# Kernel optimization log

Hardware: AMD Instinct MI355X
Metric: run time of the kernel (lower is better)

Reference implementation:

```python
import jax, jax.numpy as jnp
import numpy as np

P = 256        # number of graph pairs
LMAX = 32      # max graph size (padded to LMAX+1 incl. virtual node)
F = 2048       # num_input_features
E = 256        # embedding_dim
INF = 10000.0


def _lengths():
    i = np.arange(P)
    len_s = 8 + (i % 25)
    len_t = 8 + ((7 * i + 3) % 25)
    return len_s.astype(np.int32), len_t.astype(np.int32)


def setup_inputs() -> dict:
    key = jax.random.key(0)
    ks = jax.random.split(key, 6)
    len_s_np, len_t_np = _lengths()
    Ns, Nt = int(len_s_np.sum()), int(len_t_np.sum())
    x_s = jax.random.normal(ks[0], (Ns, F), jnp.float32)
    x_t = jax.random.normal(ks[1], (Nt, F), jnp.float32)
    W1 = jax.random.normal(ks[2], (E, F), jnp.float32) / np.float32(np.sqrt(F))
    b1 = jnp.zeros((E,), jnp.float32)
    W2 = jax.random.normal(ks[3], (E, E), jnp.float32) / np.float32(np.sqrt(E))
    b2 = jnp.zeros((E,), jnp.float32)
    virtual_embedding = jax.random.uniform(ks[4], (F,), jnp.float32)
    return {"x_s": x_s, "x_t": x_t, "W1": W1, "b1": b1, "W2": W2, "b2": b2,
            "virtual_embedding": virtual_embedding,
            "len_s": jnp.asarray(len_s_np), "len_t": jnp.asarray(len_t_np)}


def _embed(x, W1, b1, W2, b2):
    # nn.Sequential(Linear, Dropout(eval=identity), ReLU, Linear, ReLU)
    h = jax.nn.relu(x @ W1.T + b1)
    return jax.nn.relu(h @ W2.T + b2)


def _safe_cdist(a, b):
    # a: [P,L,E], b: [P,L,E] -> [P,L,L] Euclidean, grad-safe at 0
    sq = (jnp.sum(a * a, -1)[:, :, None] + jnp.sum(b * b, -1)[:, None, :]
          - 2.0 * jnp.einsum('pid,pjd->pij', a, b))
    sq = jnp.maximum(sq, 0.0)
    pos = sq > 0
    return jnp.where(pos, jnp.sqrt(jnp.where(pos, sq, 1.0)), 0.0)


def _pad_embed(emb, virtual_e, lens):
    # ragged [N,E] -> padded [P,LMAX+1,E]; slot lens[p] (and beyond) = virtual
    pos = jnp.arange(LMAX + 1)
    off = jnp.cumsum(lens) - lens                       # exclusive prefix sum
    idx = off[:, None] + jnp.minimum(pos[None, :], lens[:, None] - 1)
    mask = pos[None, :] < lens[:, None]
    return jnp.where(mask[..., None], emb[idx], virtual_e[None, None, :])


def _edit_costs(x_s, x_t, W1, b1, W2, b2, virtual_embedding, len_s, len_t):
    emb_s = _embed(x_s, W1, b1, W2, b2)
    emb_t = _embed(x_t, W1, b1, W2, b2)
    ve = _embed(virtual_embedding[None, :], W1, b1, W2, b2)[0]
    A = _pad_embed(emb_s, ve, len_s)                    # [P,L+1,E]
    B = _pad_embed(emb_t, ve, len_t)
    d = _safe_cdist(A, B)                               # [P,L+1,L+1]
    pos = jnp.arange(LMAX + 1)
    valid = ((pos[None, :, None] <= len_s[:, None, None]) &
             (pos[None, None, :] <= len_t[:, None, None]))
    tot = jnp.sum(jnp.where(valid, d, 0.0), axis=(1, 2))
    scale = (len_s * len_t).astype(d.dtype) / tot
    return jnp.where(valid, d * scale[:, None, None], 0.0), valid


def _lap_jv(C):
    # Jonker-Volgenant / e-maxx Hungarian for square cost matrix; returns col of each row
    C = np.asarray(C, dtype=np.float64)
    n = C.shape[0]
    u = np.zeros(n + 1)
    v = np.zeros(n + 1)
    p = np.zeros(n + 1, dtype=np.int64)
    way = np.zeros(n + 1, dtype=np.int64)
    for i in range(1, n + 1):
        p[0] = i
        j0 = 0
        minv = np.full(n + 1, np.inf)
        used = np.zeros(n + 1, dtype=bool)
        while True:
            used[j0] = True
            i0 = p[j0]
            cur = C[i0 - 1, :] - u[i0] - v[1:]
            upd = (~used[1:]) & (cur < minv[1:])
            minv[1:][upd] = cur[upd]
            way[1:][upd] = j0
            masked = np.where(used[1:], np.inf, minv[1:])
            j1 = int(np.argmin(masked)) + 1
            delta = masked[j1 - 1]
            u[p[used]] += delta
            v[used] -= delta
            minv[1:][~used[1:]] -= delta
            j0 = j1
            if p[j0] == 0:
                break
        while j0:
            j1 = way[j0]
            p[j0] = p[j1]
            j0 = j1
    row_of_col = p[1:] - 1
    col_of_row = np.empty(n, dtype=np.int64)
    col_of_row[row_of_col] = np.arange(n)
    return col_of_row


def _lsape_align(ec, n, m):
    # LSAPE expansion identical to GEDModelHomology.lsape
    N = n + m
    C = np.zeros((N, N))
    C[:n, :m] = ec[:n, :m]
    C[n:, :m] = INF
    C[:n, m:] = INF
    C[np.arange(n, n + m), np.arange(m)] = ec[n, :m]
    C[np.arange(n), np.arange(m, m + n)] = ec[:n, m]
    C[~np.isfinite(C)] = INF
    p = _lap_jv(C)
    q = np.arange(N)
    align = np.zeros((n + 1, m + 1), dtype=np.int32)
    align[np.minimum(q, n), np.minimum(p, m)] = 1
    align[-1, -1] = 0
    return align


def _alignments(costs_np, len_s_np, len_t_np):
    out = np.zeros((costs_np.shape[0], LMAX + 1, LMAX + 1), dtype=np.int32)
    for pr in range(costs_np.shape[0]):
        n, m = int(len_s_np[pr]), int(len_t_np[pr])
        out[pr, :n + 1, :m + 1] = _lsape_align(costs_np[pr, :n + 1, :m + 1], n, m)
    return out


def reference(x_s, x_t, W1, b1, W2, b2, virtual_embedding, len_s, len_t):
    costs, _ = _edit_costs(x_s, x_t, W1, b1, W2, b2, virtual_embedding, len_s, len_t)
    aligns = jnp.asarray(_alignments(np.asarray(costs),
                                     np.asarray(len_s), np.asarray(len_t)))
    geds = (jnp.sum(aligns.astype(costs.dtype) * costs, axis=(1, 2))
            / (len_s + len_t).astype(costs.dtype))
    return aligns, costs, geds
```

## Files before the change

kernel.cpp:

```cpp
#include <hip/hip_runtime.h>
#include <math.h>

#define LMAXP1 33
#define EDIM   256
#define FBIG   3.0e38f

typedef _Float16 half8 __attribute__((ext_vector_type(8)));
typedef float    f32x4 __attribute__((ext_vector_type(4)));

__device__ inline unsigned pk2h(_Float16 a, _Float16 b) {
    union { _Float16 h[2]; unsigned u; } q; q.h[0] = a; q.h[1] = b; return q.u;
}

__global__ __launch_bounds__(256)
void k_convw(const float* __restrict__ W, unsigned* __restrict__ Wh,
             unsigned* __restrict__ Wl, int npairs) {
    const int stride = gridDim.x * blockDim.x;
    for (int i = blockIdx.x * blockDim.x + threadIdx.x; i < npairs; i += stride) {
        const float a0 = W[2*i] * 1024.0f, a1 = W[2*i+1] * 1024.0f;
        const _Float16 h0 = (_Float16)a0, h1 = (_Float16)a1;
        const _Float16 l0 = (_Float16)(a0 - (float)h0);
        const _Float16 l1 = (_Float16)(a1 - (float)h1);
        Wh[i] = pk2h(h0, h1); Wl[i] = pk2h(l0, l1);
    }
}

#define ASTR 20
__global__ __launch_bounds__(256)
void k_gemm_splitk(const float* __restrict__ S0, int n0,
                   const float* __restrict__ S1, int n1,
                   const float* __restrict__ S2,
                   const unsigned* __restrict__ Wh, const unsigned* __restrict__ Wl,
                   float* __restrict__ Part, int Mtot, int K, int kchunk) {
    __shared__ alignas(16) unsigned AsH[64 * ASTR],  AsL[64 * ASTR];
    __shared__ alignas(16) unsigned BsH[256 * ASTR], BsL[256 * ASTR];
    const int tid = threadIdx.x;
    const int m0  = blockIdx.x * 64;
    const int ks  = blockIdx.z;
    const int kb  = ks * kchunk;
    const int ke  = (kb + kchunk < K) ? kb + kchunk : K;

    const int sar = tid >> 2, sak = (tid & 3) << 3;
    const int gr  = m0 + sar;
    const float* srow = nullptr;
    if (gr < n0)            srow = S0 + (size_t)gr * K;
    else if (gr < n0 + n1)  srow = S1 + (size_t)(gr - n0) * K;
    else if (gr < Mtot)     srow = S2;

    const int lane = tid & 63, wv = tid >> 6;
    const int wc = wv << 6;
    const int lr = lane & 15, lq = lane >> 4;

    f32x4 acc[4][4] = {};

    for (int k0 = kb; k0 < ke; k0 += 32) {
        {
            float x[8];
            if (srow) {
                const float4 f0 = *(const float4*)(srow + k0 + sak + 0);
                const float4 f1 = *(const float4*)(srow + k0 + sak + 4);
                x[0]=f0.x; x[1]=f0.y; x[2]=f0.z; x[3]=f0.w;
                x[4]=f1.x; x[5]=f1.y; x[6]=f1.z; x[7]=f1.w;
            } else {
                #pragma unroll
                for (int j = 0; j < 8; ++j) x[j] = 0.f;
            }
            unsigned uh[4], ul[4];
            #pragma unroll
            for (int j = 0; j < 4; ++j) {
                const _Float16 h0 = (_Float16)x[2*j],   h1 = (_Float16)x[2*j+1];
                const _Float16 l0 = (_Float16)(x[2*j]   - (float)h0);
                const _Float16 l1 = (_Float16)(x[2*j+1] - (float)h1);
                uh[j] = pk2h(h0, h1); ul[j] = pk2h(l0, l1);
            }
            *(uint4*)(AsH + sar * ASTR + (sak >> 1)) = make_uint4(uh[0],uh[1],uh[2],uh[3]);
            *(uint4*)(AsL + sar * ASTR + (sak >> 1)) = make_uint4(ul[0],ul[1],ul[2],ul[3]);
        }
        #pragma unroll
        for (int it = 0; it < 4; ++it) {
            const int idx = tid + it * 256;
            const int br = idx >> 2, bk = (idx & 3) << 3;
            const size_t uoff = (size_t)br * (K >> 1) + ((k0 + bk) >> 1);
            *(uint4*)(BsH + br * ASTR + (bk >> 1)) = *(const uint4*)(Wh + uoff);
            *(uint4*)(BsL + br * ASTR + (bk >> 1)) = *(const uint4*)(Wl + uoff);
        }
        __syncthreads();

        half8 bhv[4], blv[4];
        #pragma unroll
        for (int ct = 0; ct < 4; ++ct) {
            const int br = wc + ct * 16 + lr;
            bhv[ct] = *(const half8*)((const char*)BsH + br * 80 + lq * 16);
            blv[ct] = *(const half8*)((const char*)BsL + br * 80 + lq * 16);
        }
        #pragma unroll
        for (int rt = 0; rt < 4; ++rt) {
            const int ar = rt * 16 + lr;
            const half8 ah = *(const half8*)((const char*)AsH + ar * 80 + lq * 16);
            const half8 al = *(const half8*)((const char*)AsL + ar * 80 + lq * 16);
            #pragma unroll
            for (int ct = 0; ct < 4; ++ct) {
                acc[rt][ct] = __builtin_amdgcn_mfma_f32_16x16x32_f16(ah, bhv[ct], acc[rt][ct], 0, 0, 0);
                acc[rt][ct] = __builtin_amdgcn_mfma_f32_16x16x32_f16(ah, blv[ct], acc[rt][ct], 0, 0, 0);
                acc[rt][ct] = __builtin_amdgcn_mfma_f32_16x16x32_f16(al, bhv[ct], acc[rt][ct], 0, 0, 0);
            }
        }
        __syncthreads();
    }

    float* pout = Part + (size_t)ks * ((size_t)Mtot * EDIM);
    const float sc = 1.0f / 1024.0f;
    #pragma unroll
    for (int rt = 0; rt < 4; ++rt) {
        #pragma unroll
        for (int r = 0; r < 4; ++r) {
            const int grr = m0 + rt * 16 + lq * 4 + r;
            if (grr >= Mtot) continue;
            #pragma unroll
            for (int ct = 0; ct < 4; ++ct)
                pout[(size_t)grr * EDIM + wc + ct * 16 + lr] = acc[rt][ct][r] * sc;
        }
    }
}

__global__ __launch_bounds__(256)
void k_reduce_bias_relu(const float* __restrict__ Part,
                        const float* __restrict__ bias,
                        unsigned* __restrict__ Hh, unsigned* __restrict__ Hl,
                        int S, size_t MN4) {
    const size_t i = (size_t)blockIdx.x * blockDim.x + threadIdx.x;
    const size_t stride = (size_t)gridDim.x * blockDim.x;
    const size_t MN = MN4 * 4;
    for (size_t i4 = i; i4 < MN4; i4 += stride) {
        float4 s = ((const float4*)Part)[i4];
        for (int z = 1; z < S; ++z)
            { const float4 q = ((const float4*)(Part + (size_t)z * MN))[i4];
              s.x += q.x; s.y += q.y; s.z += q.z; s.w += q.w; }
        const float4 b = ((const float4*)bias)[i4 & 63];
        s.x = fmaxf(s.x + b.x, 0.f); s.y = fmaxf(s.y + b.y, 0.f);
        s.z = fmaxf(s.z + b.z, 0.f); s.w = fmaxf(s.w + b.w, 0.f);
        const _Float16 hx = (_Float16)s.x, hy = (_Float16)s.y;
        const _Float16 hz = (_Float16)s.z, hw = (_Float16)s.w;
        Hh[i4*2+0] = pk2h(hx, hy);
        Hh[i4*2+1] = pk2h(hz, hw);
        Hl[i4*2+0] = pk2h((_Float16)(s.x - (float)hx), (_Float16)(s.y - (float)hy));
        Hl[i4*2+1] = pk2h((_Float16)(s.z - (float)hz), (_Float16)(s.w - (float)hw));
    }
}

__global__ __launch_bounds__(256)
void k_gemm_f16(const unsigned* __restrict__ Ah, const unsigned* __restrict__ Al,
                const unsigned* __restrict__ Wh, const unsigned* __restrict__ Wl,
                const float* __restrict__ bias,
                float* __restrict__ C, int Mtot, int K) {
    __shared__ alignas(16) unsigned AsH[64 * ASTR],  AsL[64 * ASTR];
    __shared__ alignas(16) unsigned BsH[256 * ASTR], BsL[256 * ASTR];
    const int tid = threadIdx.x;
    const int m0  = blockIdx.x * 64;

    const int sar = tid >> 2, sak = (tid & 3) << 3;
    const int gr  = m0 + sar;
    const bool arow = (gr < Mtot);

    const int lane = tid & 63, wv = tid >> 6;
    const int wc = wv << 6;
    const int lr = lane & 15, lq = lane >> 4;

    f32x4 acc[4][4] = {};

    for (int k0 = 0; k0 < K; k0 += 32) {
        {
            uint4 vh = make_uint4(0,0,0,0), vl = vh;
            if (arow) {
                const size_t uoff = (size_t)gr * (K >> 1) + ((k0 + sak) >> 1);
                vh = *(const uint4*)(Ah + uoff);
                vl = *(const uint4*)(Al + uoff);
            }
            *(uint4*)(AsH + sar * ASTR + (sak >> 1)) = vh;
            *(uint4*)(AsL + sar * ASTR + (sak >> 1)) = vl;
        }
        #pragma unroll
        for (int it = 0; it < 4; ++it) {
            const int idx = tid + it * 256;
            const int br = idx >> 2, bk = (idx & 3) << 3;
            const size_t uoff = (size_t)br * (K >> 1) + ((k0 + bk) >> 1);
            *(uint4*)(BsH + br * ASTR + (bk >> 1)) = *(const uint4*)(Wh + uoff);
            *(uint4*)(BsL + br * ASTR + (bk >> 1)) = *(const uint4*)(Wl + uoff);
        }
        __syncthreads();

        half8 bhv[4], blv[4];
        #pragma unroll
        for (int ct = 0; ct < 4; ++ct) {
            const int br = wc + ct * 16 + lr;
            bhv[ct] = *(const half8*)((const char*)BsH + br * 80 + lq * 16);
            blv[ct] = *(const half8*)((const char*)BsL + br * 80 + lq * 16);
        }
        #pragma unroll
        for (int rt = 0; rt < 4; ++rt) {
            const int ar = rt * 16 + lr;
            const half8 ah = *(const half8*)((const char*)AsH + ar * 80 + lq * 16);
            const half8 al = *(const half8*)((const char*)AsL + ar * 80 + lq * 16);
            #pragma unroll
            for (int ct = 0; ct < 4; ++ct) {
                acc[rt][ct] = __builtin_amdgcn_mfma_f32_16x16x32_f16(ah, bhv[ct], acc[rt][ct], 0, 0, 0);
                acc[rt][ct] = __builtin_amdgcn_mfma_f32_16x16x32_f16(ah, blv[ct], acc[rt][ct], 0, 0, 0);
                acc[rt][ct] = __builtin_amdgcn_mfma_f32_16x16x32_f16(al, bhv[ct], acc[rt][ct], 0, 0, 0);
            }
        }
        __syncthreads();
    }

    const float sc = 1.0f / 1024.0f;
    #pragma unroll
    for (int rt = 0; rt < 4; ++rt) {
        #pragma unroll
        for (int r = 0; r < 4; ++r) {
            const int grr = m0 + rt * 16 + lq * 4 + r;
            if (grr >= Mtot) continue;
            #pragma unroll
            for (int ct = 0; ct < 4; ++ct) {
                const int gc = wc + ct * 16 + lr;
                C[(size_t)grr * EDIM + gc] = fmaxf(acc[rt][ct][r] * sc + bias[gc], 0.0f);
            }
        }
    }
}

__global__ __launch_bounds__(256)
void k_embed_gemm(const float* __restrict__ S0, int n0,
                  const float* __restrict__ S1, int n1,
                  const float* __restrict__ S2,
                  const float* __restrict__ W, const float* __restrict__ bias,
                  float* __restrict__ C, int Mtot, int K) {
    __shared__ alignas(16) float As[16][68];
    __shared__ alignas(16) float Bs[16][68];
    const int tid  = threadIdx.x;
    const int tx   = tid & 15, ty = tid >> 4;
    const int m0   = blockIdx.x * 64, nc0 = blockIdx.y * 64;
    const int lrow = tid >> 2;
    const int lk4  = (tid & 3) << 2;

    const int gr = m0 + lrow;
    const float* srow = nullptr;
    if (gr < n0)            srow = S0 + (size_t)gr * K;
    else if (gr < n0 + n1)  srow = S1 + (size_t)(gr - n0) * K;
    else if (gr < Mtot)     srow = S2;
    const float* wrow = W + (size_t)(nc0 + lrow) * K;

    float acc[4][4] = {};
    for (int k0 = 0; k0 < K; k0 += 16) {
        float4 va = make_float4(0.f, 0.f, 0.f, 0.f);
        if (srow) va = *(const float4*)(srow + k0 + lk4);
        const float4 vb = *(const float4*)(wrow + k0 + lk4);
        As[lk4+0][lrow] = va.x; As[lk4+1][lrow] = va.y;
        As[lk4+2][lrow] = va.z; As[lk4+3][lrow] = va.w;
        Bs[lk4+0][lrow] = vb.x; Bs[lk4+1][lrow] = vb.y;
        Bs[lk4+2][lrow] = vb.z; Bs[lk4+3][lrow] = vb.w;
        __syncthreads();
        #pragma unroll
        for (int kk = 0; kk < 16; ++kk) {
            const float4 a4 = *(const float4*)&As[kk][ty << 2];
            const float4 b4 = *(const float4*)&Bs[kk][tx << 2];
            const float av[4] = {a4.x, a4.y, a4.z, a4.w};
            const float bv[4] = {b4.x, b4.y, b4.z, b4.w};
            #pragma unroll
            for (int i2 = 0; i2 < 4; ++i2)
                #pragma unroll
                for (int j2 = 0; j2 < 4; ++j2)
                    acc[i2][j2] = fmaf(av[i2], bv[j2], acc[i2][j2]);
        }
        __syncthreads();
    }
    #pragma unroll
    for (int i2 = 0; i2 < 4; ++i2) {
        const int grr = m0 + (ty << 2) + i2;
        if (grr >= Mtot) continue;
        #pragma unroll
        for (int j2 = 0; j2 < 4; ++j2) {
            const int gc = nc0 + (tx << 2) + j2;
            const float vv = acc[i2][j2] + bias[gc];
            C[(size_t)grr * EDIM + gc] = fmaxf(vv, 0.0f);
        }
    }
}

#define CSTR 36
__global__ __launch_bounds__(256)
void k_costs(const float* __restrict__ Emb, const int* __restrict__ len_s,
             const int* __restrict__ len_t, int Ns, int Nt,
             float* __restrict__ costs) {
    __shared__ alignas(16) unsigned Ah[34 * CSTR], Al[34 * CSTR];
    __shared__ alignas(16) unsigned Bh[34 * CSTR], Bl[34 * CSTR];
    __shared__ float dtile[LMAXP1 * LMAXP1];
    __shared__ float na[LMAXP1], nb[LMAXP1];
    __shared__ float red[256];
    __shared__ float s_scale;
    const int p = blockIdx.x, tid = threadIdx.x;
    const int n = len_s[p], m = len_t[p];
    int offs = 0, offt = 0;
    for (int j = 0; j < p; ++j) { offs += len_s[j]; offt += len_t[j]; }
    const int veRow = Ns + Nt;
    const int tbase = Ns + offt;

    const int lane = tid & 63, wv = tid >> 6;
    const int lr = lane & 15, lq = lane >> 4;

    if (tid <= n) {
        const float* src = (tid < n) ? (Emb + (size_t)(offs + tid) * EDIM)
                                     : (Emb + (size_t)veRow * EDIM);
        const float4* a4 = (const float4*)src;
        float s = 0.f;
        for (int k = 0; k < 64; ++k) {
            const float4 a = a4[k];
            s = fmaf(a.x, a.x, s); s = fmaf(a.y, a.y, s);
            s = fmaf(a.z, a.z, s); s = fmaf(a.w, a.w, s);
        }
        na[tid] = s;
    } else if (tid >= 64 && tid - 64 <= m) {
        const int j = tid - 64;
        const float* src = (j < m) ? (Emb + (size_t)(tbase + j) * EDIM)
                                   : (Emb + (size_t)veRow * EDIM);
        const float4* b4 = (const float4*)src;
        float s = 0.f;
        for (int k = 0; k < 64; ++k) {
            const float4 b = b4[k];
            s = fmaf(b.x, b.x, s); s = fmaf(b.y, b.y, s);
            s = fmaf(b.z, b.z, s); s = fmaf(b.w, b.w, s);
        }
        nb[j] = s;
    }

    f32x4 g0 = {}, g1 = {}, g2 = {};
    const int t0 = wv, t1 = wv + 4, t2 = wv + 8;

    for (int k0 = 0; k0 < EDIM; k0 += 64) {
        for (int idx = tid; idx < 34 * 16; idx += 256) {
            const int r = idx >> 4, c4 = idx & 15;
            float4 va = make_float4(0.f,0.f,0.f,0.f), vb = va;
            if (r < n)       va = *(const float4*)(Emb + (size_t)(offs + r) * EDIM + k0 + c4*4);
            else if (r == n) va = *(const float4*)(Emb + (size_t)veRow * EDIM + k0 + c4*4);
            if (r < m)       vb = *(const float4*)(Emb + (size_t)(tbase + r) * EDIM + k0 + c4*4);
            else if (r == m) vb = *(const float4*)(Emb + (size_t)veRow * EDIM + k0 + c4*4);
            const float xa[4] = {va.x, va.y, va.z, va.w};
            const float xb[4] = {vb.x, vb.y, vb.z, vb.w};
            unsigned ah_[2], al_[2], bh_[2], bl_[2];
            #pragma unroll
            for (int j = 0; j < 2; ++j) {
                const _Float16 h0 = (_Float16)xa[2*j],   h1 = (_Float16)xa[2*j+1];
                const _Float16 l0 = (_Float16)(xa[2*j]   - (float)h0);
                const _Float16 l1 = (_Float16)(xa[2*j+1] - (float)h1);
                ah_[j] = pk2h(h0, h1); al_[j] = pk2h(l0, l1);
                const _Float16 g0_ = (_Float16)xb[2*j],   g1_ = (_Float16)xb[2*j+1];
                const _Float16 m0_ = (_Float16)(xb[2*j]   - (float)g0_);
                const _Float16 m1_ = (_Float16)(xb[2*j+1] - (float)g1_);
                bh_[j] = pk2h(g0_, g1_); bl_[j] = pk2h(m0_, m1_);
            }
            const int uo = r * CSTR + c4 * 2;
            *(uint2*)(Ah + uo) = make_uint2(ah_[0], ah_[1]);
            *(uint2*)(Al + uo) = make_uint2(al_[0], al_[1]);
            *(uint2*)(Bh + uo) = make_uint2(bh_[0], bh_[1]);
            *(uint2*)(Bl + uo) = make_uint2(bl_[0], bl_[1]);
        }
        __syncthreads();

        #pragma unroll
        for (int kf = 0; kf < 2; ++kf) {
#define GRAM_TILE(T, G) { \
            const int tr_ = (T) / 3, tc_ = (T) % 3;                              \
            const int ar_ = tr_ * 16 + lr, br_ = tc_ * 16 + lr;                  \
            const half8 ah = *(const half8*)((const char*)Ah + ar_*144 + kf*64 + lq*16); \
            const half8 al = *(const half8*)((const char*)Al + ar_*144 + kf*64 + lq*16); \
            const half8 bh = *(const half8*)((const char*)Bh + br_*144 + kf*64 + lq*16); \
            const half8 bl = *(const half8*)((const char*)Bl + br_*144 + kf*64 + lq*16); \
            G = __builtin_amdgcn_mfma_f32_16x16x32_f16(ah, bh, G, 0, 0, 0);      \
            G = __builtin_amdgcn_mfma_f32_16x16x32_f16(ah, bl, G, 0, 0, 0);      \
            G = __builtin_amdgcn_mfma_f32_16x16x32_f16(al, bh, G, 0, 0, 0); }
            GRAM_TILE(t0, g0)
            GRAM_TILE(t1, g1)
            if (wv == 0) GRAM_TILE(t2, g2)
#undef GRAM_TILE
        }
        __syncthreads();
    }

#define DTILE_OUT(T, G) { \
    const int tr_ = (T) / 3, tc_ = (T) % 3;                                      \
    _Pragma("unroll")                                                            \
    for (int r = 0; r < 4; ++r) {                                                \
        const int i_ = tr_ * 16 + lq * 4 + r, j_ = tc_ * 16 + lr;                \
        if (i_ <= n && j_ <= m) {                                                \
            const float sq = fmaxf(na[i_] + nb[j_] - 2.0f * G[r], 0.0f);         \
            dtile[i_ * LMAXP1 + j_] = (sq > 0.0f) ? sqrtf(sq) : 0.0f;            \
        } } }
    DTILE_OUT(t0, g0)
    DTILE_OUT(t1, g1)
    if (wv == 0) DTILE_OUT(t2, g2)
#undef DTILE_OUT
    __syncthreads();

    float lsum = 0.f;
    const int m1 = m + 1;
    const int cells = (n + 1) * m1;
    for (int c = tid; c < cells; c += 256) {
        const int i = c / m1, j = c - i * m1;
        lsum += dtile[i * LMAXP1 + j];
    }
    red[tid] = lsum;
    __syncthreads();
    for (int s = 128; s > 0; s >>= 1) {
        if (tid < s) red[tid] += red[tid + s];
        __syncthreads();
    }
    if (tid == 0) s_scale = (float)(n * m) / red[0];
    __syncthreads();
    const float scale = s_scale;
    for (int idx = tid; idx < LMAXP1 * LMAXP1; idx += 256) {
        const int i = idx / LMAXP1, j = idx - i * LMAXP1;
        const float v = (i <= n && j <= m) ? dtile[i * LMAXP1 + j] * scale : 0.0f;
        costs[(size_t)p * (LMAXP1 * LMAXP1) + idx] = v;
    }
}

__device__ inline int rdlane_i(int v, int l) { return __builtin_amdgcn_readlane(v, l); }
__device__ inline float rdlane_f(float v, int l) {
    return __int_as_float(__builtin_amdgcn_readlane(__float_as_int(v), l));
}
__device__ inline unsigned wave_umin64(unsigned x) {
#define DPPMINU(ctrl) { unsigned t_ = (unsigned)__builtin_amdgcn_update_dpp(  \
        (int)x, (int)x, (ctrl), 0xf, 0xf, false);                             \
        x = (t_ < x) ? t_ : x; }
    DPPMINU(0xB1)
    DPPMINU(0x4E)
    DPPMINU(0x141)
    DPPMINU(0x140)
    DPPMINU(0x142)
    DPPMINU(0x143)
#undef DPPMINU
    return (unsigned)__builtin_amdgcn_readlane((int)x, 63);
}

__global__ __launch_bounds__(64)
void k_lap(const float* __restrict__ costs, const int* __restrict__ len_s,
           const int* __restrict__ len_t, float* __restrict__ aligns,
           float* __restrict__ geds) {
    __shared__ float ec[LMAXP1 * LMAXP1];
    __shared__ float Ms[33 * 64];
    const int p = blockIdx.x, lane = threadIdx.x;
    const int n = len_s[p], m = len_t[p];
    const float* cp = costs + (size_t)p * (LMAXP1 * LMAXP1);
    for (int idx = lane; idx < LMAXP1 * LMAXP1; idx += 64) ec[idx] = cp[idx];
    __syncthreads();

    const bool swp = (n > m);
    const int R  = swp ? n : m;
    const int S_ = swp ? m : n;
    const bool vec = (lane >= 1 && lane <= R);

    for (int r = 1; r <= R; ++r) {
        float cv = FBIG;
        const int i0b = r - 1, j0b = lane - 1;
        if (vec) {
            if (!swp) {
                const float ins = ec[n * LMAXP1 + j0b];
                cv = (i0b < S_)
                   ? fminf(ec[i0b * LMAXP1 + j0b], ec[i0b * LMAXP1 + m] + ins)
                   : ins;
            } else {
                const float ins = ec[j0b * LMAXP1 + m];
                cv = (i0b < S_)
                   ? fminf(ec[j0b * LMAXP1 + i0b], ec[n * LMAXP1 + i0b] + ins)
                   : ins;
            }
        }
        Ms[(r << 6) + lane] = cv;
    }
    __syncthreads();

    float v_l = 0.0f;
    int amin_l = 0;
    if (vec) {
        float best = FBIG;
        for (int r = 1; r <= R; ++r) {
            const float c = Ms[(r << 6) + lane];
            if (c < best) { best = c; amin_l = r; }
        }
        v_l = best;
    }
    int p_l = 0;
    unsigned long long rowfree = ((1ull << R) - 1ull) << 1;
    for (int j = 1; j <= R; ++j) {
        const int ai = rdlane_i(amin_l, j);
        if ((rowfree >> ai) & 1ull) {
            if (lane == j) p_l = ai;
            rowfree &= ~(1ull << ai);
        }
    }

    float ucol = 0.0f, minv_l = FBIG;
    int way_l = 0;

    for (int i = 1; i <= R; ++i) {
        if (!((rowfree >> i) & 1ull)) continue;
        if (lane == 0) { p_l = i; ucol = 0.0f; }
        minv_l = FBIG;
        int used_l = 0;
        int j0 = 0, i0 = i;
        float u_i0 = 0.0f;
        while (true) {
            if (lane == j0) used_l = 1;
            const float cur = Ms[(i0 << 6) + lane] - u_i0 - v_l;
            const bool unused = vec && !used_l;
            if (unused && cur < minv_l) { minv_l = cur; way_l = j0; }
            const float mval = unused ? fmaxf(minv_l, 0.0f) : FBIG;
            const unsigned key = (__float_as_uint(mval) & ~63u) | (unsigned)lane;
            const unsigned kmin = wave_umin64(key);
            const int j1 = (int)(kmin & 63u);
            const float delta = rdlane_f(minv_l, j1);
            if (used_l) { ucol += delta; v_l -= delta; }
            if (unused) minv_l -= delta;
            j0 = j1;
            i0 = rdlane_i(p_l, j1);
            u_i0 = rdlane_f(ucol, j1);
            if (i0 == 0) break;
        }
        int jj = j0;
        while (jj != 0) {
            const int   j1a = rdlane_i(way_l, jj);
            const int   pn  = rdlane_i(p_l, j1a);
            const float un  = rdlane_f(ucol, j1a);
            if (lane == jj) { p_l = pn; ucol = un; }
            jj = j1a;
        }
    }

    float* ap = aligns + (size_t)p * (LMAXP1 * LMAXP1);
    for (int idx = lane; idx < LMAXP1 * LMAXP1; idx += 64) ap[idx] = 0.0f;
    __syncthreads();
    float gedv = 0.0f;
    if (vec) {
        const int i0b = p_l - 1;
        const int j0b = lane - 1;
        if (!swp) {
            if (i0b < S_) {
                const float sub = ec[i0b * LMAXP1 + j0b];
                const float alt = ec[i0b * LMAXP1 + m] + ec[n * LMAXP1 + j0b];
                if (sub <= alt) { ap[i0b * LMAXP1 + j0b] = 1.0f; gedv = sub; }
                else { ap[i0b * LMAXP1 + m] = 1.0f;
                       ap[n * LMAXP1 + j0b] = 1.0f;
                       gedv = alt; }
            } else {
                ap[n * LMAXP1 + j0b] = 1.0f;
                gedv = ec[n * LMAXP1 + j0b];
            }
        } else {
            if (i0b < S_) {
                const float sub = ec[j0b * LMAXP1 + i0b];
                const float alt = ec[n * LMAXP1 + i0b] + ec[j0b * LMAXP1 + m];
                if (sub <= alt) { ap[j0b * LMAXP1 + i0b] = 1.0f; gedv = sub; }
                else { ap[n * LMAXP1 + i0b] = 1.0f;
                       ap[j0b * LMAXP1 + m] = 1.0f;
                       gedv = alt; }
            } else {
                ap[j0b * LMAXP1 + m] = 1.0f;
                gedv = ec[j0b * LMAXP1 + m];
            }
        }
    }
    #pragma unroll
    for (int off = 32; off > 0; off >>= 1) gedv += __shfl_xor(gedv, off);
    if (lane == 0) geds[p] = gedv / (float)(n + m);
}

extern "C" void kernel_launch(void* const* d_in, const int* in_sizes, int n_in,
                              void* d_out, int out_size, void* d_ws, size_t ws_size,
                              hipStream_t stream) {
    const float* x_s = (const float*)d_in[0];
    const float* x_t = (const float*)d_in[1];
    const float* W1  = (const float*)d_in[2];
    const float* b1  = (const float*)d_in[3];
    const float* W2  = (const float*)d_in[4];
    const float* b2  = (const float*)d_in[5];
    const float* ve  = (const float*)d_in[6];
    const int* len_s = (const int*)d_in[7];
    const int* len_t = (const int*)d_in[8];
    const int P    = in_sizes[7];
    const int Ns   = in_sizes[0] / 2048;
    const int Nt   = in_sizes[1] / 2048;
    const int Mtot = Ns + Nt + 1;
    const size_t MN  = (size_t)Mtot * EDIM;

    float* out_aligns = (float*)d_out;
    float* out_costs  = out_aligns + (size_t)P * LMAXP1 * LMAXP1;
    float* out_geds   = out_costs  + (size_t)P * LMAXP1 * LMAXP1;

    const dim3 b256(256);
    const int gx64 = (Mtot + 63) / 64;

    const size_t fixed = MN  + 2 * 262144 + 2 * 32768;
    int S = 0;
    if (ws_size >= (4 * MN + fixed) * sizeof(float)) S = 4;
    else if (ws_size >= (2 * MN + fixed) * sizeof(float)) S = 2;

    if (S > 0) {
        float* Part = (float*)d_ws;
        float* Emb  = Part;
        unsigned* Hh  = (unsigned*)(Part + (size_t)S * MN);
        unsigned* Hl  = Hh + MN / 2;
        unsigned* W1h = Hl + MN / 2;
        unsigned* W1l = W1h + 262144;
        unsigned* W2h = W1l + 262144;
        unsigned* W2l = W2h + 32768;

        k_convw<<<dim3(1024), b256, 0, stream>>>(W1, W1h, W1l, 262144);
        k_convw<<<dim3(128),  b256, 0, stream>>>(W2, W2h, W2l, 32768);

        k_gemm_splitk<<<dim3(gx64, 1, S), b256, 0, stream>>>(
            x_s, Ns, x_t, Nt, ve, W1h, W1l, Part, Mtot, 2048, 2048 / S);

        const size_t MN4 = MN / 4;
        const int rblocks = (int)((MN4 + 255) / 256) < 2048
                          ? (int)((MN4 + 255) / 256) : 2048;
        k_reduce_bias_relu<<<dim3(rblocks), b256, 0, stream>>>(Part, b1, Hh, Hl, S, MN4);

        k_gemm_f16<<<dim3(gx64), b256, 0, stream>>>(Hh, Hl, W2h, W2l, b2, Emb, Mtot, 256);

        k_costs<<<dim3(P), b256, 0, stream>>>(Emb, len_s, len_t, Ns, Nt, out_costs);
        k_lap<<<dim3(P), dim3(64), 0, stream>>>(out_costs, len_s, len_t, out_aligns, out_geds);
    } else {
        float* H   = (float*)d_ws;
        float* Emb = H + MN;
        k_embed_gemm<<<dim3(gx64, 4), b256, 0, stream>>>(
            x_s, Ns, x_t, Nt, ve, W1, b1, H, Mtot, 2048);
        k_embed_gemm<<<dim3(gx64, 4), b256, 0, stream>>>(
            H, Mtot, nullptr, 0, nullptr, W2, b2, Emb, Mtot, 256);
        k_costs<<<dim3(P), b256, 0, stream>>>(Emb, len_s, len_t, Ns, Nt, out_costs);
        k_lap<<<dim3(P), dim3(64), 0, stream>>>(out_costs, len_s, len_t, out_aligns, out_geds);
    }
}
```

Before: 174.9 us.

## Emit split-f16 embeddings from GEMM, precompute norms, keep LAP cost rows in registers

The second embedding GEMM now writes the hi/lo f16 split of its output directly, and a new small kernel computes per-row squared norms once. The costs kernel then loads the pre-split halves instead of reconverting fp32 per pair and recomputing norms, which cuts repeated global reads and conversion work. Separately, the LAP kernel keeps each lane's cost column in a 32-entry register array and selects a row with a mux tree, replacing shared-memory lookups. The changes add a kernel launch and extra workspace, and the register array raises register pressure in the LAP kernel.

```diff
diff --git a/kernel.cpp b/kernel.cpp
--- a/kernel.cpp
+++ b/kernel.cpp
@@ -14,15 +14,38 @@
 
 __global__ __launch_bounds__(256)
 void k_convw(const float* __restrict__ W, unsigned* __restrict__ Wh,
-             unsigned* __restrict__ Wl, int npairs) {
+             unsigned* __restrict__ Wl, int npairs, float scale) {
     const int stride = gridDim.x * blockDim.x;
     for (int i = blockIdx.x * blockDim.x + threadIdx.x; i < npairs; i += stride) {
-        const float a0 = W[2*i] * 1024.0f, a1 = W[2*i+1] * 1024.0f;
+        const float a0 = W[2*i] * scale, a1 = W[2*i+1] * scale;
         const _Float16 h0 = (_Float16)a0, h1 = (_Float16)a1;
         const _Float16 l0 = (_Float16)(a0 - (float)h0);
         const _Float16 l1 = (_Float16)(a1 - (float)h1);
         Wh[i] = pk2h(h0, h1); Wl[i] = pk2h(l0, l1);
     }
+}
+
+__global__ __launch_bounds__(256)
+void k_norms(const unsigned* __restrict__ Eh, const unsigned* __restrict__ El,
+             float* __restrict__ Norms, int Mtot) {
+    const int row  = blockIdx.x * 4 + (threadIdx.x >> 6);
+    const int lane = threadIdx.x & 63;
+    if (row >= Mtot) return;
+    const uint2 h2 = *(const uint2*)(Eh + (size_t)row * 128 + lane * 2);
+    const uint2 l2 = *(const uint2*)(El + (size_t)row * 128 + lane * 2);
+    union { unsigned u; _Float16 h[2]; } qh, ql;
+    float s = 0.f;
+    qh.u = h2.x; ql.u = l2.x;
+    { const float x0 = (float)qh.h[0] + (float)ql.h[0];
+      const float x1 = (float)qh.h[1] + (float)ql.h[1];
+      s = fmaf(x0, x0, s); s = fmaf(x1, x1, s); }
+    qh.u = h2.y; ql.u = l2.y;
+    { const float x0 = (float)qh.h[0] + (float)ql.h[0];
+      const float x1 = (float)qh.h[1] + (float)ql.h[1];
+      s = fmaf(x0, x0, s); s = fmaf(x1, x1, s); }
+    #pragma unroll
+    for (int off = 32; off > 0; off >>= 1) s += __shfl_xor(s, off);
+    if (lane == 0) Norms[row] = s;
 }
 
 #define ASTR 20
@@ -152,7 +175,8 @@
 void k_gemm_f16(const unsigned* __restrict__ Ah, const unsigned* __restrict__ Al,
                 const unsigned* __restrict__ Wh, const unsigned* __restrict__ Wl,
                 const float* __restrict__ bias,
-                float* __restrict__ C, int Mtot, int K) {
+                unsigned* __restrict__ Eh, unsigned* __restrict__ El,
+                int Mtot, int K) {
     __shared__ alignas(16) unsigned AsH[64 * ASTR],  AsL[64 * ASTR];
     __shared__ alignas(16) unsigned BsH[256 * ASTR], BsL[256 * ASTR];
     const int tid = threadIdx.x;
@@ -211,6 +235,8 @@
         __syncthreads();
     }
 
+    _Float16* ph = (_Float16*)Eh;
+    _Float16* pl = (_Float16*)El;
     const float sc = 1.0f / 1024.0f;
     #pragma unroll
     for (int rt = 0; rt < 4; ++rt) {
@@ -221,7 +247,10 @@
             #pragma unroll
             for (int ct = 0; ct < 4; ++ct) {
                 const int gc = wc + ct * 16 + lr;
-                C[(size_t)grr * EDIM + gc] = fmaxf(acc[rt][ct][r] * sc + bias[gc], 0.0f);
+                const float vv = fmaxf(acc[rt][ct][r] * sc + bias[gc], 0.0f);
+                const _Float16 hv = (_Float16)vv;
+                ph[(size_t)grr * EDIM + gc] = hv;
+                pl[(size_t)grr * EDIM + gc] = (_Float16)(vv - (float)hv);
             }
         }
     }
@@ -287,9 +316,10 @@
 
 #define CSTR 36
 __global__ __launch_bounds__(256)
-void k_costs(const float* __restrict__ Emb, const int* __restrict__ len_s,
-             const int* __restrict__ len_t, int Ns, int Nt,
-             float* __restrict__ costs) {
+void k_costs(const unsigned* __restrict__ Eh, const unsigned* __restrict__ El,
+             const float* __restrict__ Norms,
+             const int* __restrict__ len_s, const int* __restrict__ len_t,
+             int Ns, int Nt, float* __restrict__ costs) {
     __shared__ alignas(16) unsigned Ah[34 * CSTR], Al[34 * CSTR];
     __shared__ alignas(16) unsigned Bh[34 * CSTR], Bl[34 * CSTR];
     __shared__ float dtile[LMAXP1 * LMAXP1];
@@ -306,30 +336,8 @@
     const int lane = tid & 63, wv = tid >> 6;
     const int lr = lane & 15, lq = lane >> 4;
 
-    if (tid <= n) {
-        const float* src = (tid < n) ? (Emb + (size_t)(offs + tid) * EDIM)
-                                     : (Emb + (size_t)veRow * EDIM);
-        const float4* a4 = (const float4*)src;
-        float s = 0.f;
-        for (int k = 0; k < 64; ++k) {
-            const float4 a = a4[k];
-            s = fmaf(a.x, a.x, s); s = fmaf(a.y, a.y, s);
-            s = fmaf(a.z, a.z, s); s = fmaf(a.w, a.w, s);
-        }
-        na[tid] = s;
-    } else if (tid >= 64 && tid - 64 <= m) {
-        const int j = tid - 64;
-        const float* src = (j < m) ? (Emb + (size_t)(tbase + j) * EDIM)
-                                   : (Emb + (size_t)veRow * EDIM);
-        const float4* b4 = (const float4*)src;
-        float s = 0.f;
-        for (int k = 0; k < 64; ++k) {
-            const float4 b = b4[k];
-            s = fmaf(b.x, b.x, s); s = fmaf(b.y, b.y, s);
-            s = fmaf(b.z, b.z, s); s = fmaf(b.w, b.w, s);
-        }
-        nb[j] = s;
-    }
+    if (tid <= n)                       na[tid] = Norms[(tid < n) ? offs + tid : veRow];
+    else if (tid >= 64 && tid - 64 <= m) nb[tid - 64] = Norms[(tid - 64 < m) ? tbase + tid - 64 : veRow];
 
     f32x4 g0 = {}, g1 = {}, g2 = {};
     const int t0 = wv, t1 = wv + 4, t2 = wv + 8;
@@ -337,30 +345,20 @@
     for (int k0 = 0; k0 < EDIM; k0 += 64) {
         for (int idx = tid; idx < 34 * 16; idx += 256) {
             const int r = idx >> 4, c4 = idx & 15;
-            float4 va = make_float4(0.f,0.f,0.f,0.f), vb = va;
-            if (r < n)       va = *(const float4*)(Emb + (size_t)(offs + r) * EDIM + k0 + c4*4);
-            else if (r == n) va = *(const float4*)(Emb + (size_t)veRow * EDIM + k0 + c4*4);
-            if (r < m)       vb = *(const float4*)(Emb + (size_t)(tbase + r) * EDIM + k0 + c4*4);
-            else if (r == m) vb = *(const float4*)(Emb + (size_t)veRow * EDIM + k0 + c4*4);
-            const float xa[4] = {va.x, va.y, va.z, va.w};
-            const float xb[4] = {vb.x, vb.y, vb.z, vb.w};
-            unsigned ah_[2], al_[2], bh_[2], bl_[2];
-            #pragma unroll
-            for (int j = 0; j < 2; ++j) {
-                const _Float16 h0 = (_Float16)xa[2*j],   h1 = (_Float16)xa[2*j+1];
-                const _Float16 l0 = (_Float16)(xa[2*j]   - (float)h0);
-                const _Float16 l1 = (_Float16)(xa[2*j+1] - (float)h1);
-                ah_[j] = pk2h(h0, h1); al_[j] = pk2h(l0, l1);
-                const _Float16 g0_ = (_Float16)xb[2*j],   g1_ = (_Float16)xb[2*j+1];
-                const _Float16 m0_ = (_Float16)(xb[2*j]   - (float)g0_);
-                const _Float16 m1_ = (_Float16)(xb[2*j+1] - (float)g1_);
-                bh_[j] = pk2h(g0_, g1_); bl_[j] = pk2h(m0_, m1_);
+            const int rowA = (r < n) ? offs + r : ((r == n) ? veRow : -1);
+            const int rowB = (r < m) ? tbase + r : ((r == m) ? veRow : -1);
+            uint2 vah = make_uint2(0,0), val = vah, vbh = vah, vbl = vah;
+            if (rowA >= 0) {
+                const size_t uo_ = (size_t)rowA * 128 + (k0 >> 1) + c4 * 2;
+                vah = *(const uint2*)(Eh + uo_); val = *(const uint2*)(El + uo_);
+            }
+            if (rowB >= 0) {
+                const size_t uo_ = (size_t)rowB * 128 + (k0 >> 1) + c4 * 2;
+                vbh = *(const uint2*)(Eh + uo_); vbl = *(const uint2*)(El + uo_);
             }
             const int uo = r * CSTR + c4 * 2;
-            *(uint2*)(Ah + uo) = make_uint2(ah_[0], ah_[1]);
-            *(uint2*)(Al + uo) = make_uint2(al_[0], al_[1]);
-            *(uint2*)(Bh + uo) = make_uint2(bh_[0], bh_[1]);
-            *(uint2*)(Bl + uo) = make_uint2(bl_[0], bl_[1]);
+            *(uint2*)(Ah + uo) = vah; *(uint2*)(Al + uo) = val;
+            *(uint2*)(Bh + uo) = vbh; *(uint2*)(Bl + uo) = vbl;
         }
         __syncthreads();
 
@@ -445,7 +443,6 @@
            const int* __restrict__ len_t, float* __restrict__ aligns,
            float* __restrict__ geds) {
     __shared__ float ec[LMAXP1 * LMAXP1];
-    __shared__ float Ms[33 * 64];
     const int p = blockIdx.x, lane = threadIdx.x;
     const int n = len_s[p], m = len_t[p];
     const float* cp = costs + (size_t)p * (LMAXP1 * LMAXP1);
@@ -457,10 +454,12 @@
     const int S_ = swp ? m : n;
     const bool vec = (lane >= 1 && lane <= R);
 
-    for (int r = 1; r <= R; ++r) {
+    float Mc[32];
+    #pragma unroll
+    for (int r = 1; r <= 32; ++r) {
         float cv = FBIG;
-        const int i0b = r - 1, j0b = lane - 1;
-        if (vec) {
+        if (vec && r <= R) {
+            const int i0b = r - 1, j0b = lane - 1;
             if (!swp) {
                 const float ins = ec[n * LMAXP1 + j0b];
                 cv = (i0b < S_)
@@ -473,17 +472,19 @@
                    : ins;
             }
         }
-        Ms[(r << 6) + lane] = cv;
-    }
-    __syncthreads();
+        Mc[r - 1] = cv;
+    }
 
     float v_l = 0.0f;
     int amin_l = 0;
     if (vec) {
         float best = FBIG;
-        for (int r = 1; r <= R; ++r) {
-            const float c = Ms[(r << 6) + lane];
-            if (c < best) { best = c; amin_l = r; }
+        #pragma unroll
+        for (int r = 1; r <= 32; ++r) {
+            if (r <= R) {
+                const float c = Mc[r - 1];
+                if (c < best) { best = c; amin_l = r; }
+            }
         }
         v_l = best;
     }
@@ -509,7 +510,22 @@
         float u_i0 = 0.0f;
         while (true) {
             if (lane == j0) used_l = 1;
-            const float cur = Ms[(i0 << 6) + lane] - u_i0 - v_l;
+            const int si = i0 - 1;
+            float s16[16];
+            #pragma unroll
+            for (int t = 0; t < 16; ++t) s16[t] = (si & 1) ? Mc[2*t+1] : Mc[2*t];
+            float s8[8];
+            #pragma unroll
+            for (int t = 0; t < 8; ++t)  s8[t]  = (si & 2) ? s16[2*t+1] : s16[2*t];
+            float s4[4];
+            #pragma unroll
+            for (int t = 0; t < 4; ++t)  s4[t]  = (si & 4) ? s8[2*t+1] : s8[2*t];
+            float s2[2];
+            #pragma unroll
+            for (int t = 0; t < 2; ++t)  s2[t]  = (si & 8) ? s4[2*t+1] : s4[2*t];
+            const float Crow = (si & 16) ? s2[1] : s2[0];
+
+            const float cur = Crow - u_i0 - v_l;
             const bool unused = vec && !used_l;
             if (unused && cur < minv_l) { minv_l = cur; way_l = j0; }
             const float mval = unused ? fmaxf(minv_l, 0.0f) : FBIG;
@@ -596,24 +612,27 @@
 
     const dim3 b256(256);
     const int gx64 = (Mtot + 63) / 64;
-
-    const size_t fixed = MN  + 2 * 262144 + 2 * 32768;
+    const int gnorm = (Mtot + 3) / 4;
+
+    const size_t fixed = MN + 10240 + 2 * 262144 + 2 * 32768;
     int S = 0;
     if (ws_size >= (4 * MN + fixed) * sizeof(float)) S = 4;
     else if (ws_size >= (2 * MN + fixed) * sizeof(float)) S = 2;
 
     if (S > 0) {
         float* Part = (float*)d_ws;
-        float* Emb  = Part;
+        unsigned* Eh  = (unsigned*)Part;
+        unsigned* El  = Eh + MN / 2;
         unsigned* Hh  = (unsigned*)(Part + (size_t)S * MN);
         unsigned* Hl  = Hh + MN / 2;
-        unsigned* W1h = Hl + MN / 2;
+        float* Norms  = (float*)(Hl + MN / 2);
+        unsigned* W1h = (unsigned*)(Norms + 10240);
         unsigned* W1l = W1h + 262144;
         unsigned* W2h = W1l + 262144;
         unsigned* W2l = W2h + 32768;
 
-        k_convw<<<dim3(1024), b256, 0, stream>>>(W1, W1h, W1l, 262144);
-        k_convw<<<dim3(128),  b256, 0, stream>>>(W2, W2h, W2l, 32768);
+        k_convw<<<dim3(1024), b256, 0, stream>>>(W1, W1h, W1l, 262144, 1024.0f);
+        k_convw<<<dim3(128),  b256, 0, stream>>>(W2, W2h, W2l, 32768, 1024.0f);
 
         k_gemm_splitk<<<dim3(gx64, 1, S), b256, 0, stream>>>(
             x_s, Ns, x_t, Nt, ve, W1h, W1l, Part, Mtot, 2048, 2048 / S);
@@ -623,18 +642,24 @@
                           ? (int)((MN4 + 255) / 256) : 2048;
         k_reduce_bias_relu<<<dim3(rblocks), b256, 0, stream>>>(Part, b1, Hh, Hl, S, MN4);
 
-        k_gemm_f16<<<dim3(gx64), b256, 0, stream>>>(Hh, Hl, W2h, W2l, b2, Emb, Mtot, 256);
-
-        k_costs<<<dim3(P), b256, 0, stream>>>(Emb, len_s, len_t, Ns, Nt, out_costs);
+        k_gemm_f16<<<dim3(gx64), b256, 0, stream>>>(Hh, Hl, W2h, W2l, b2, Eh, El, Mtot, 256);
+        k_norms<<<dim3(gnorm), b256, 0, stream>>>(Eh, El, Norms, Mtot);
+
+        k_costs<<<dim3(P), b256, 0, stream>>>(Eh, El, Norms, len_s, len_t, Ns, Nt, out_costs);
         k_lap<<<dim3(P), dim3(64), 0, stream>>>(out_costs, len_s, len_t, out_aligns, out_geds);
     } else {
         float* H   = (float*)d_ws;
         float* Emb = H + MN;
+        unsigned* Eh = (unsigned*)(Emb + MN);
+        unsigned* El = Eh + MN / 2;
+        float* Norms = (float*)(El + MN / 2);
         k_embed_gemm<<<dim3(gx64, 4), b256, 0, stream>>>(
             x_s, Ns, x_t, Nt, ve, W1, b1, H, Mtot, 2048);
         k_embed_gemm<<<dim3(gx64, 4), b256, 0, stream>>>(
             H, Mtot, nullptr, 0, nullptr, W2, b2, Emb, Mtot, 256);
-        k_costs<<<dim3(P), b256, 0, stream>>>(Emb, len_s, len_t, Ns, Nt, out_costs);
+        k_convw<<<dim3(1024), b256, 0, stream>>>(Emb, Eh, El, (int)(MN / 2), 1.0f);
+        k_norms<<<dim3(gnorm), b256, 0, stream>>>(Eh, El, Norms, Mtot);
+        k_costs<<<dim3(P), b256, 0, stream>>>(Eh, El, Norms, len_s, len_t, Ns, Nt, out_costs);
         k_lap<<<dim3(P), dim3(64), 0, stream>>>(out_costs, len_s, len_t, out_aligns, out_geds);
     }
 }
```

After: 358.8 us. 2.05x slower.
